# Performance work log

Measured on AMD Instinct MI355X. Metric: run time of the kernel, lower is better.

The kernel has to match this reference:

```python
import jax, jax.numpy as jnp
import numpy as np

H = 16      # num_heads
D = 64      # head_dim
BQ = 64     # block_size_q
BKV = 64    # block_size_kv


def setup_inputs() -> dict:
    key = jax.random.key(0)
    ks = jax.random.split(key, 5)
    B, S, dim = 2, 2048, 1024
    x = jax.random.normal(ks[0], (B, S, dim), dtype=jnp.float32)
    Wq = jax.random.normal(ks[1], (dim, H * D), dtype=jnp.float32) * 0.02
    Wk = jax.random.normal(ks[2], (dim, H * D), dtype=jnp.float32) * 0.02
    Wv = jax.random.normal(ks[3], (dim, H * D), dtype=jnp.float32) * 0.02
    Wo = jax.random.normal(ks[4], (H * D, dim), dtype=jnp.float32) * 0.02
    return {"x": x, "Wq": Wq, "Wk": Wk, "Wv": Wv, "Wo": Wo}


def _flash_tiled(q, k, v, scale):
    # q,k,v: (B, H, S, D). Non-causal tiled attention with online softmax,
    # faithfully replicating the source's per-iteration division by l_new.
    B, nh, S, d = q.shape
    nq, nkv = S // BQ, S // BKV
    qb = q.reshape(B, nh, nq, BQ, d)                       # all q blocks at once (outer loop vectorized)
    kb = k.reshape(B, nh, nkv, BKV, d).transpose(2, 0, 1, 3, 4)  # (nkv, B, H, BKV, D)
    vb = v.reshape(B, nh, nkv, BKV, d).transpose(2, 0, 1, 3, 4)

    o0 = jnp.zeros((B, nh, nq, BQ, d), q.dtype)
    m0 = jnp.full((B, nh, nq, BQ), -jnp.inf, q.dtype)
    l0 = jnp.zeros((B, nh, nq, BQ), q.dtype)

    def step(carry, kv):
        o, m, l = carry
        kj, vj = kv
        s = jnp.einsum('bhnqd,bhkd->bhnqk', qb, kj) * scale   # (B,H,nq,BQ,BKV)
        m_new = jnp.maximum(m, s.max(axis=-1))
        p = jnp.exp(s - m_new[..., None])
        alpha = jnp.exp(m - m_new)
        l_new = alpha * l + p.sum(axis=-1)
        # NOTE: division by l_new every iteration, as in the source module.
        o_new = (alpha[..., None] * o + jnp.einsum('bhnqk,bhkd->bhnqd', p, vj)) / l_new[..., None]
        return (o_new, m_new, l_new), None

    (o, _, _), _ = jax.lax.scan(step, (o0, m0, l0), (kb, vb))
    return o.reshape(B, nh, S, d)


def reference(x, Wq, Wk, Wv, Wo):
    B, S, dim = x.shape
    scale = D ** -0.5
    q = (x @ Wq).reshape(B, S, H, D).transpose(0, 2, 1, 3)
    k = (x @ Wk).reshape(B, S, H, D).transpose(0, 2, 1, 3)
    v = (x @ Wv).reshape(B, S, H, D).transpose(0, 2, 1, 3)
    o = _flash_tiled(q, k, v, scale)                       # (B,H,S,D)
    out = o.transpose(0, 2, 1, 3).reshape(B, S, H * D)
    return out @ Wo
```

## Files before the change

kernel.cpp:

```cpp
#include <hip/hip_runtime.h>
#include <hip/hip_bf16.h>
#include <math.h>

#define BB   2
#define SS   2048
#define DIM  1024
#define NH   16
#define HD   64
#define MTOT (BB * SS)

typedef unsigned short ushortT;
typedef __attribute__((ext_vector_type(8))) short short8v;
typedef __attribute__((ext_vector_type(4))) float float4v;

union FragU { short8v v; unsigned short us[8]; unsigned int u[4]; };

__device__ inline unsigned short f2bf(float x) {
    unsigned u = __builtin_bit_cast(unsigned, x);
    u += 0x7fffu + ((u >> 16) & 1u);
    return (unsigned short)(u >> 16);
}
__device__ inline float bf2f(unsigned short h) {
    unsigned u = ((unsigned)h) << 16;
    return __builtin_bit_cast(float, u);
}
__device__ inline void split_tr(float x, unsigned short& hi, unsigned short& lo) {
    unsigned u = __builtin_bit_cast(unsigned, x);
    hi = (unsigned short)(u >> 16);
    float hf = __builtin_bit_cast(float, u & 0xffff0000u);
    lo = (unsigned short)(__builtin_bit_cast(unsigned, x - hf) >> 16);
}
__device__ inline void split4(const float4& x, short4& hi, short4& lo) {
    unsigned short h0 = f2bf(x.x), h1 = f2bf(x.y), h2 = f2bf(x.z), h3 = f2bf(x.w);
    hi = make_short4((short)h0, (short)h1, (short)h2, (short)h3);
    lo = make_short4((short)f2bf(x.x - bf2f(h0)), (short)f2bf(x.y - bf2f(h1)),
                     (short)f2bf(x.z - bf2f(h2)), (short)f2bf(x.w - bf2f(h3)));
}
__device__ inline void gld_lds16(const void* g, void* l) {
    __builtin_amdgcn_global_load_lds(
        (const __attribute__((address_space(1))) void*)g,
        (__attribute__((address_space(3))) void*)l, 16, 0, 0);
}

__global__ __launch_bounds__(256) void convert_split_kernel(
    const float* __restrict__ in, ushortT* __restrict__ hi, ushortT* __restrict__ lo, int n4)
{
    int t = blockIdx.x * 256 + threadIdx.x;
    if (t < n4) {
        float4 x = ((const float4*)in)[t];
        short4 h, l; split4(x, h, l);
        ((short4*)hi)[t] = h;
        ((short4*)lo)[t] = l;
    }
}

__global__ __launch_bounds__(256) void transpose_split_kernel(
    const float* __restrict__ W0, const float* __restrict__ W1,
    const float* __restrict__ W2, const float* __restrict__ W3,
    ushortT* __restrict__ WtH, ushortT* __restrict__ WtL)
{
    const int z = blockIdx.z;
    const float* __restrict__ W = (z == 0) ? W0 : (z == 1) ? W1 : (z == 2) ? W2 : W3;
    ushortT* H = WtH + (size_t)z * 1024 * 1024;
    ushortT* L = WtL + (size_t)z * 1024 * 1024;

    __shared__ float T[64][65];
    const int k0 = blockIdx.y * 64, n0 = blockIdx.x * 64;
    const int tid = threadIdx.x;
    const int c4 = (tid & 15) * 4;

#pragma unroll
    for (int i = 0; i < 4; i++) {
        int r = (tid >> 4) + 16 * i;
        *(float4*)&T[r][c4] = *(const float4*)(W + (size_t)(k0 + r) * 1024 + n0 + c4);
    }
    __syncthreads();
#pragma unroll
    for (int i = 0; i < 4; i++) {
        int n = (tid >> 4) + 16 * i;
        float4 vv = make_float4(T[c4 + 0][n], T[c4 + 1][n], T[c4 + 2][n], T[c4 + 3][n]);
        short4 h, l; split4(vv, h, l);
        *(short4*)&H[(size_t)(n0 + n) * 1024 + k0 + c4] = h;
        *(short4*)&L[(size_t)(n0 + n) * 1024 + k0 + c4] = l;
    }
}

__global__ __launch_bounds__(256) void kv_convert_kernel(
    const float* __restrict__ kw,
    ushortT* __restrict__ KhG, ushortT* __restrict__ KlG)
{
    const int jb = blockIdx.x, bh = blockIdx.y;
    const int b = bh >> 4, h = bh & 15;

    __shared__ float T[64][68];
    const int tid = threadIdx.x;
    const size_t ibase = (size_t)b * SS * DIM + (size_t)h * HD + (size_t)(jb * 64) * DIM;
    const int c4 = (tid & 15) * 4;
#pragma unroll
    for (int i = 0; i < 4; i++) {
        int r = (tid >> 4) + 16 * i;
        *(float4*)&T[r][c4] = *(const float4*)(kw + ibase + (size_t)r * DIM + c4);
    }
    __syncthreads();

    ushortT* oh = KhG + (size_t)(bh * 32 + jb) * 4096;
    ushortT* ol = KlG + (size_t)(bh * 32 + jb) * 4096;

#pragma unroll
    for (int i = 0; i < 2; i++) {
        const int s = tid + i * 256;
        const int f = s >> 6;
        const int lane = s & 63;
        const int ks = f >> 2, c = f & 3;
        const int qd = lane >> 4, l15 = lane & 15;
        const int kv = c * 16 + l15;
        const int d0 = ks * 32 + qd * 8;
        ushortT hv[8], lv[8];
#pragma unroll
        for (int j = 0; j < 8; j++) split_tr(T[kv][d0 + j], hv[j], lv[j]);
        *(short4*)&oh[s * 8]     = *(short4*)&hv[0];
        *(short4*)&oh[s * 8 + 4] = *(short4*)&hv[4];
        *(short4*)&ol[s * 8]     = *(short4*)&lv[0];
        *(short4*)&ol[s * 8 + 4] = *(short4*)&lv[4];
    }
}

__global__ __launch_bounds__(256, 3) void gemm_bt_split_kernel(
    const ushortT* __restrict__ Ah, const ushortT* __restrict__ Al,
    const ushortT* __restrict__ BtH, const ushortT* __restrict__ BtL,
    float* __restrict__ Y0, float* __restrict__ Y1,
    ushortT* __restrict__ VhG, ushortT* __restrict__ VlG)
{
    const int z = blockIdx.z;
    const ushortT* __restrict__ Bh = BtH + (size_t)z * 1024 * 1024;
    const ushortT* __restrict__ Bl = BtL + (size_t)z * 1024 * 1024;

    const int K = 1024, N = 1024;
    const int m0 = blockIdx.y * 128;
    const int n0 = blockIdx.x * 128;

    __shared__ __align__(16) ushortT AhS[128 * 32];
    __shared__ __align__(16) ushortT AlS[128 * 32];
    __shared__ __align__(16) ushortT BhS[128 * 32];
    __shared__ __align__(16) ushortT BlS[128 * 32];

    const int tid  = threadIdx.x;
    const int wave = tid >> 6, lane = tid & 63;
    const int quad = lane >> 4, l15 = lane & 15;
    const int wm = wave >> 1, wn = wave & 1;

    const int s0 = tid, s1 = tid + 256;
    const int ar0 = s0 >> 2, ak0 = (s0 & 3) * 8;
    const int ar1 = s1 >> 2, ak1 = (s1 & 3) * 8;

    float4v acc[4][4];
#pragma unroll
    for (int i = 0; i < 4; i++)
#pragma unroll
        for (int j = 0; j < 4; j++) acc[i][j] = (float4v){0.f, 0.f, 0.f, 0.f};

    for (int k0 = 0; k0 < K; k0 += 32) {
        __syncthreads();
        gld_lds16(Ah + (size_t)(m0 + ar0) * K + k0 + ak0, &AhS[s0 * 8]);
        gld_lds16(Ah + (size_t)(m0 + ar1) * K + k0 + ak1, &AhS[s1 * 8]);
        gld_lds16(Al + (size_t)(m0 + ar0) * K + k0 + ak0, &AlS[s0 * 8]);
        gld_lds16(Al + (size_t)(m0 + ar1) * K + k0 + ak1, &AlS[s1 * 8]);
        gld_lds16(Bh + (size_t)(n0 + ar0) * K + k0 + ak0, &BhS[s0 * 8]);
        gld_lds16(Bh + (size_t)(n0 + ar1) * K + k0 + ak1, &BhS[s1 * 8]);
        gld_lds16(Bl + (size_t)(n0 + ar0) * K + k0 + ak0, &BlS[s0 * 8]);
        gld_lds16(Bl + (size_t)(n0 + ar1) * K + k0 + ak1, &BlS[s1 * 8]);
        __syncthreads();

        FragU ah[4], al[4], bh[4], bl[4];
#pragma unroll
        for (int t = 0; t < 4; t++) {
            ah[t].v = *(const short8v*)&AhS[(wm * 64 + t * 16 + l15) * 32 + quad * 8];
            al[t].v = *(const short8v*)&AlS[(wm * 64 + t * 16 + l15) * 32 + quad * 8];
            bh[t].v = *(const short8v*)&BhS[(wn * 64 + t * 16 + l15) * 32 + quad * 8];
            bl[t].v = *(const short8v*)&BlS[(wn * 64 + t * 16 + l15) * 32 + quad * 8];
        }
#pragma unroll
        for (int mt = 0; mt < 4; mt++)
#pragma unroll
            for (int nt = 0; nt < 4; nt++) {
                acc[mt][nt] = __builtin_amdgcn_mfma_f32_16x16x32_bf16(ah[mt].v, bh[nt].v, acc[mt][nt], 0, 0, 0);
                acc[mt][nt] = __builtin_amdgcn_mfma_f32_16x16x32_bf16(ah[mt].v, bl[nt].v, acc[mt][nt], 0, 0, 0);
                acc[mt][nt] = __builtin_amdgcn_mfma_f32_16x16x32_bf16(al[mt].v, bh[nt].v, acc[mt][nt], 0, 0, 0);
            }
    }

    if (z == 2) {
        const int b  = m0 >> 11;
        const int jb = ((m0 & 2047) >> 6) + wm;
        const int h  = (n0 >> 6) + wn;
        const size_t tb = (size_t)((b * 16 + h) * 32 + jb) * 4096;
        ushortT* vh = VhG + tb;
        ushortT* vl = VlG + tb;
#pragma unroll
        for (int mt = 0; mt < 4; mt++)
#pragma unroll
            for (int nt = 0; nt < 4; nt++) {
                const int off = ((((mt >> 1) * 4 + nt) * 64 +
                                  ((mt & 1) * 2 + (quad >> 1)) * 16 + l15) * 8) +
                                (quad & 1) * 4;
                short4 hi, lo;
                float4 vv = make_float4(acc[mt][nt][0], acc[mt][nt][1],
                                        acc[mt][nt][2], acc[mt][nt][3]);
                unsigned short h0, l0, h1, l1, h2, l2, h3, l3;
                split_tr(vv.x, h0, l0); split_tr(vv.y, h1, l1);
                split_tr(vv.z, h2, l2); split_tr(vv.w, h3, l3);
                hi = make_short4((short)h0, (short)h1, (short)h2, (short)h3);
                lo = make_short4((short)l0, (short)l1, (short)l2, (short)l3);
                *(short4*)&vh[off] = hi;
                *(short4*)&vl[off] = lo;
            }
    } else {
        float* __restrict__ Y = (z == 0) ? Y0 : Y1;
#pragma unroll
        for (int mt = 0; mt < 4; mt++)
#pragma unroll
            for (int r = 0; r < 4; r++) {
                const int row = m0 + wm * 64 + mt * 16 + quad * 4 + r;
                float* yp = Y + (size_t)row * N + n0 + wn * 64 + l15;
#pragma unroll
                for (int nt = 0; nt < 4; nt++)
                    yp[nt * 16] = acc[mt][nt][r];
            }
    }
}

__global__ __launch_bounds__(256, 2) void attn_mfma_kernel(
    const float* __restrict__ q,
    const ushortT* __restrict__ KhG, const ushortT* __restrict__ KlG,
    const ushortT* __restrict__ VhG, const ushortT* __restrict__ VlG,
    ushortT* __restrict__ Oh, ushortT* __restrict__ Ol)
{
    __shared__ __align__(16) ushortT KhS[4096];
    __shared__ __align__(16) ushortT KlS[4096];
    __shared__ __align__(16) ushortT VhS[4096];
    __shared__ __align__(16) ushortT VlS[4096];
    __shared__ __align__(16) ushortT PW[4][2][2048];

    const int tid  = threadIdx.x;
    const int wave = tid >> 6, lane = tid & 63;
    const int quad = lane >> 4, l15 = lane & 15;
    const int bh = blockIdx.y, b = bh >> 4, h = bh & 15;
    const size_t base = (size_t)b * SS * DIM + (size_t)h * HD;
    const int qs0 = blockIdx.x * 128 + wave * 32;

    const float qscale = 0.125f * 1.4426950408889634f;
    FragU Qh[2][2], Ql[2][2];
#pragma unroll
    for (int rt = 0; rt < 2; rt++) {
        const int qrow = qs0 + rt * 16 + l15;
#pragma unroll
        for (int ks = 0; ks < 2; ks++) {
            const float* p0 = q + base + (size_t)qrow * DIM + ks * 32 + quad * 8;
            float4 a = *(const float4*)(p0);
            float4 c = *(const float4*)(p0 + 4);
            float e[8] = {a.x, a.y, a.z, a.w, c.x, c.y, c.z, c.w};
#pragma unroll
            for (int j = 0; j < 8; j++) {
                float x = e[j] * qscale;
                unsigned short hs = f2bf(x);
                Qh[rt][ks].us[j] = hs;
                Ql[rt][ks].us[j] = f2bf(x - bf2f(hs));
            }
        }
    }

    float4v Oacc[4][2];
#pragma unroll
    for (int dt = 0; dt < 4; dt++)
#pragma unroll
        for (int rt = 0; rt < 2; rt++) Oacc[dt][rt] = (float4v){0.f, 0.f, 0.f, 0.f};

    float m_run[2] = {-INFINITY, -INFINITY};
    float l_run[2] = {0.f, 0.f};

    const int sl0 = wave * 128 + lane, sl1 = sl0 + 64;
    ushortT* ph = &PW[wave][0][0];
    ushortT* pl = &PW[wave][1][0];
    const int pwq = ((quad >> 1) * 16 + l15) * 8 + (quad & 1) * 4;
    const int lane8 = lane * 8;

    for (int jb = 0; jb < 32; jb++) {
        __syncthreads();
        {
            const size_t tb = (size_t)(bh * 32 + jb) * 4096;
            gld_lds16(KhG + tb + sl0 * 8, &KhS[sl0 * 8]);
            gld_lds16(KhG + tb + sl1 * 8, &KhS[sl1 * 8]);
            gld_lds16(KlG + tb + sl0 * 8, &KlS[sl0 * 8]);
            gld_lds16(KlG + tb + sl1 * 8, &KlS[sl1 * 8]);
            gld_lds16(VhG + tb + sl0 * 8, &VhS[sl0 * 8]);
            gld_lds16(VhG + tb + sl1 * 8, &VhS[sl1 * 8]);
            gld_lds16(VlG + tb + sl0 * 8, &VlS[sl0 * 8]);
            gld_lds16(VlG + tb + sl1 * 8, &VlS[sl1 * 8]);
        }
        __syncthreads();

        float4v st[4][2];
#pragma unroll
        for (int mt = 0; mt < 4; mt++)
#pragma unroll
            for (int rt = 0; rt < 2; rt++) st[mt][rt] = (float4v){0.f, 0.f, 0.f, 0.f};

#pragma unroll
        for (int ks = 0; ks < 2; ks++) {
            FragU kh[4], kl[4];
#pragma unroll
            for (int mt = 0; mt < 4; mt++) {
                kh[mt].v = *(const short8v*)&KhS[((ks * 4 + mt) * 64) * 8 + lane8];
                kl[mt].v = *(const short8v*)&KlS[((ks * 4 + mt) * 64) * 8 + lane8];
            }
#pragma unroll
            for (int mt = 0; mt < 4; mt++)
#pragma unroll
                for (int rt = 0; rt < 2; rt++) {
                    st[mt][rt] = __builtin_amdgcn_mfma_f32_16x16x32_bf16(kh[mt].v, Qh[rt][ks].v, st[mt][rt], 0, 0, 0);
                    st[mt][rt] = __builtin_amdgcn_mfma_f32_16x16x32_bf16(kh[mt].v, Ql[rt][ks].v, st[mt][rt], 0, 0, 0);
                    st[mt][rt] = __builtin_amdgcn_mfma_f32_16x16x32_bf16(kl[mt].v, Qh[rt][ks].v, st[mt][rt], 0, 0, 0);
                }
        }

        float oscale[2];
#pragma unroll
        for (int rt = 0; rt < 2; rt++) {
            float v0 = fmaxf(fmaxf(st[0][rt][0], st[0][rt][1]), fmaxf(st[0][rt][2], st[0][rt][3]));
#pragma unroll
            for (int mt = 1; mt < 4; mt++) {
                float v1 = fmaxf(fmaxf(st[mt][rt][0], st[mt][rt][1]), fmaxf(st[mt][rt][2], st[mt][rt][3]));
                v0 = fmaxf(v0, v1);
            }
            v0 = fmaxf(v0, __shfl_xor(v0, 16, 64));
            v0 = fmaxf(v0, __shfl_xor(v0, 32, 64));
            const float mn = fmaxf(m_run[rt], v0);
            const float al = __builtin_amdgcn_exp2f(m_run[rt] - mn);

            float ssum = 0.f;
#pragma unroll
            for (int mt = 0; mt < 4; mt++)
#pragma unroll
                for (int r = 0; r < 4; r++) {
                    const float p = __builtin_amdgcn_exp2f(st[mt][rt][r] - mn);
                    st[mt][rt][r] = p;
                    ssum += p;
                }
            ssum += __shfl_xor(ssum, 16, 64);
            ssum += __shfl_xor(ssum, 32, 64);
            const float ln = al * l_run[rt] + ssum;
            const float inv = __builtin_amdgcn_rcpf(ln);
            oscale[rt] = al * inv;
#pragma unroll
            for (int mt = 0; mt < 4; mt++)
#pragma unroll
                for (int r = 0; r < 4; r++)
                    st[mt][rt][r] *= inv;
            m_run[rt] = mn;
            l_run[rt] = ln;
        }

#pragma unroll
        for (int rt = 0; rt < 2; rt++)
#pragma unroll
            for (int mt = 0; mt < 4; mt++) {
                unsigned u0 = __builtin_bit_cast(unsigned, st[mt][rt][0]);
                unsigned u1 = __builtin_bit_cast(unsigned, st[mt][rt][1]);
                unsigned u2 = __builtin_bit_cast(unsigned, st[mt][rt][2]);
                unsigned u3 = __builtin_bit_cast(unsigned, st[mt][rt][3]);
                unsigned h01 = (u0 >> 16) | (u1 & 0xffff0000u);
                unsigned h23 = (u2 >> 16) | (u3 & 0xffff0000u);
                float d0 = st[mt][rt][0] - __builtin_bit_cast(float, u0 & 0xffff0000u);
                float d1 = st[mt][rt][1] - __builtin_bit_cast(float, u1 & 0xffff0000u);
                float d2 = st[mt][rt][2] - __builtin_bit_cast(float, u2 & 0xffff0000u);
                float d3 = st[mt][rt][3] - __builtin_bit_cast(float, u3 & 0xffff0000u);
                unsigned l01 = (__builtin_bit_cast(unsigned, d0) >> 16) |
                               (__builtin_bit_cast(unsigned, d1) & 0xffff0000u);
                unsigned l23 = (__builtin_bit_cast(unsigned, d2) >> 16) |
                               (__builtin_bit_cast(unsigned, d3) & 0xffff0000u);
                const int idx = ((rt * 2 + (mt >> 1)) * 512 + (mt & 1) * 256) + pwq;
                *(uint2*)&ph[idx] = make_uint2(h01, h23);
                *(uint2*)&pl[idx] = make_uint2(l01, l23);
            }

        FragU Ph[2][2], Pl[2][2];
#pragma unroll
        for (int rt = 0; rt < 2; rt++)
#pragma unroll
            for (int ks = 0; ks < 2; ks++) {
                Ph[rt][ks].v = *(const short8v*)&ph[((rt * 2 + ks) * 64) * 8 + lane8];
                Pl[rt][ks].v = *(const short8v*)&pl[((rt * 2 + ks) * 64) * 8 + lane8];
            }

#pragma unroll
        for (int dt = 0; dt < 4; dt++)
#pragma unroll
            for (int rt = 0; rt < 2; rt++)
#pragma unroll
                for (int r = 0; r < 4; r++)
                    Oacc[dt][rt][r] *= oscale[rt];

#pragma unroll
        for (int ks = 0; ks < 2; ks++)
#pragma unroll
            for (int dt = 0; dt < 4; dt++) {
                FragU vh, vl;
                vh.v = *(const short8v*)&VhS[((ks * 4 + dt) * 64) * 8 + lane8];
                vl.v = *(const short8v*)&VlS[((ks * 4 + dt) * 64) * 8 + lane8];
#pragma unroll
                for (int rt = 0; rt < 2; rt++) {
                    Oacc[dt][rt] = __builtin_amdgcn_mfma_f32_16x16x32_bf16(vh.v, Ph[rt][ks].v, Oacc[dt][rt], 0, 0, 0);
                    Oacc[dt][rt] = __builtin_amdgcn_mfma_f32_16x16x32_bf16(vl.v, Ph[rt][ks].v, Oacc[dt][rt], 0, 0, 0);
                    Oacc[dt][rt] = __builtin_amdgcn_mfma_f32_16x16x32_bf16(vh.v, Pl[rt][ks].v, Oacc[dt][rt], 0, 0, 0);
                }
            }
    }

    float* Pf = (float*)&PW[wave][0][0];
    const int q16 = lane >> 2, c = lane & 3;
#pragma unroll
    for (int rt = 0; rt < 2; rt++) {
#pragma unroll
        for (int dt = 0; dt < 4; dt++)
            *(float4v*)&Pf[l15 * 68 + dt * 16 + quad * 4] = Oacc[dt][rt];
        float vals[16];
#pragma unroll
        for (int kk = 0; kk < 4; kk++)
            *(float4v*)&vals[kk * 4] = *(const float4v*)&Pf[q16 * 68 + c * 16 + kk * 4];

        unsigned ho[8], lo8[8];
#pragma unroll
        for (int kk = 0; kk < 8; kk++) {
            unsigned short h0, l0, h1, l1;
            split_tr(vals[2 * kk], h0, l0);
            split_tr(vals[2 * kk + 1], h1, l1);
            ho[kk]  = (unsigned)h0 | ((unsigned)h1 << 16);
            lo8[kk] = (unsigned)l0 | ((unsigned)l1 << 16);
        }
        const int qrow = qs0 + rt * 16 + q16;
        const size_t off = (size_t)(b * SS + qrow) * DIM + h * HD + c * 16;
        *(uint4*)&Oh[off]     = make_uint4(ho[0], ho[1], ho[2], ho[3]);
        *(uint4*)&Oh[off + 8] = make_uint4(ho[4], ho[5], ho[6], ho[7]);
        *(uint4*)&Ol[off]     = make_uint4(lo8[0], lo8[1], lo8[2], lo8[3]);
        *(uint4*)&Ol[off + 8] = make_uint4(lo8[4], lo8[5], lo8[6], lo8[7]);
    }
}

extern "C" void kernel_launch(void* const* d_in, const int* in_sizes, int n_in,
                              void* d_out, int out_size, void* d_ws, size_t ws_size,
                              hipStream_t stream)
{
    const float* x  = (const float*)d_in[0];
    const float* Wq = (const float*)d_in[1];
    const float* Wk = (const float*)d_in[2];
    const float* Wv = (const float*)d_in[3];
    const float* Wo = (const float*)d_in[4];
    float* out = (float*)d_out;

    char* w = (char*)d_ws;
    float*   qw  = (float*)(w);
    float*   kw  = (float*)(w + ((size_t)16 << 20));
    ushortT* VhG = (ushortT*)(w + ((size_t)32 << 20));
    ushortT* VlG = (ushortT*)(w + ((size_t)40 << 20));
    ushortT* XhS = (ushortT*)(w + ((size_t)48 << 20));
    ushortT* XlS = (ushortT*)(w + ((size_t)56 << 20));
    ushortT* WtH = (ushortT*)(w + ((size_t)64 << 20));
    ushortT* WtL = (ushortT*)(w + ((size_t)72 << 20));
    ushortT* KhG = (ushortT*)(w + ((size_t)80 << 20));
    ushortT* KlG = (ushortT*)(w + ((size_t)88 << 20));
    ushortT* OhS = (ushortT*)kw;
    ushortT* OlS = (ushortT*)(w + ((size_t)24 << 20));

    dim3 blk(256);
    const int n4 = MTOT * DIM / 4;

    convert_split_kernel<<<dim3(n4 / 256), blk, 0, stream>>>(x, XhS, XlS, n4);
    transpose_split_kernel<<<dim3(16, 16, 4), blk, 0, stream>>>(Wq, Wk, Wv, Wo, WtH, WtL);

    gemm_bt_split_kernel<<<dim3(8, 32, 3), blk, 0, stream>>>(
        XhS, XlS, WtH, WtL, qw, kw, VhG, VlG);

    kv_convert_kernel<<<dim3(32, 32), blk, 0, stream>>>(kw, KhG, KlG);

    attn_mfma_kernel<<<dim3(16, 32), blk, 0, stream>>>(qw, KhG, KlG, VhG, VlG, OhS, OlS);

    gemm_bt_split_kernel<<<dim3(8, 32, 1), blk, 0, stream>>>(
        OhS, OlS, WtH + (size_t)3 * 1024 * 1024, WtL + (size_t)3 * 1024 * 1024,
        out, nullptr, nullptr, nullptr);
}
```

Baseline: 333.5 us.

## Fuse K split into projection GEMM, merge prep kernels, prefetch K/V tiles

Merges the x-convert and weight-transpose kernels into one launch. Moves the K hi/lo split and fragment relayout into the QKV GEMM epilogue, using swapped MFMA operands for z==1, so the separate kv_convert kernel and the fp32 K round trip through memory go away. In the attention loop, K and V fragments are loaded into registers before a barrier, and the next tile's global-to-LDS loads are issued so they overlap the current compute. This adds register pressure and extra barriers in exchange for fewer launches, less memory traffic and latency hiding.

Measured after the change: 780.7 us. 2.34x slower.

```diff
diff --git a/kernel.cpp b/kernel.cpp
--- a/kernel.cpp
+++ b/kernel.cpp
@@ -42,31 +42,29 @@
         (__attribute__((address_space(3))) void*)l, 16, 0, 0);
 }
 
-__global__ __launch_bounds__(256) void convert_split_kernel(
-    const float* __restrict__ in, ushortT* __restrict__ hi, ushortT* __restrict__ lo, int n4)
-{
-    int t = blockIdx.x * 256 + threadIdx.x;
-    if (t < n4) {
-        float4 x = ((const float4*)in)[t];
-        short4 h, l; split4(x, h, l);
-        ((short4*)hi)[t] = h;
-        ((short4*)lo)[t] = l;
-    }
-}
-
-__global__ __launch_bounds__(256) void transpose_split_kernel(
+__global__ __launch_bounds__(256) void prep_kernel(
+    const float* __restrict__ x,
     const float* __restrict__ W0, const float* __restrict__ W1,
     const float* __restrict__ W2, const float* __restrict__ W3,
+    ushortT* __restrict__ XhS, ushortT* __restrict__ XlS,
     ushortT* __restrict__ WtH, ushortT* __restrict__ WtL)
 {
     const int z = blockIdx.z;
+    const int tid = threadIdx.x;
+    if (z >= 4) {
+        int t = (((z - 4) * 256 + blockIdx.y * 16 + blockIdx.x)) * 256 + tid;
+        float4 xv = ((const float4*)x)[t];
+        short4 h, l; split4(xv, h, l);
+        ((short4*)XhS)[t] = h;
+        ((short4*)XlS)[t] = l;
+        return;
+    }
     const float* __restrict__ W = (z == 0) ? W0 : (z == 1) ? W1 : (z == 2) ? W2 : W3;
     ushortT* H = WtH + (size_t)z * 1024 * 1024;
     ushortT* L = WtL + (size_t)z * 1024 * 1024;
 
     __shared__ float T[64][65];
     const int k0 = blockIdx.y * 64, n0 = blockIdx.x * 64;
-    const int tid = threadIdx.x;
     const int c4 = (tid & 15) * 4;
 
 #pragma unroll
@@ -85,50 +83,11 @@
     }
 }
 
-__global__ __launch_bounds__(256) void kv_convert_kernel(
-    const float* __restrict__ kw,
-    ushortT* __restrict__ KhG, ushortT* __restrict__ KlG)
-{
-    const int jb = blockIdx.x, bh = blockIdx.y;
-    const int b = bh >> 4, h = bh & 15;
-
-    __shared__ float T[64][68];
-    const int tid = threadIdx.x;
-    const size_t ibase = (size_t)b * SS * DIM + (size_t)h * HD + (size_t)(jb * 64) * DIM;
-    const int c4 = (tid & 15) * 4;
-#pragma unroll
-    for (int i = 0; i < 4; i++) {
-        int r = (tid >> 4) + 16 * i;
-        *(float4*)&T[r][c4] = *(const float4*)(kw + ibase + (size_t)r * DIM + c4);
-    }
-    __syncthreads();
-
-    ushortT* oh = KhG + (size_t)(bh * 32 + jb) * 4096;
-    ushortT* ol = KlG + (size_t)(bh * 32 + jb) * 4096;
-
-#pragma unroll
-    for (int i = 0; i < 2; i++) {
-        const int s = tid + i * 256;
-        const int f = s >> 6;
-        const int lane = s & 63;
-        const int ks = f >> 2, c = f & 3;
-        const int qd = lane >> 4, l15 = lane & 15;
-        const int kv = c * 16 + l15;
-        const int d0 = ks * 32 + qd * 8;
-        ushortT hv[8], lv[8];
-#pragma unroll
-        for (int j = 0; j < 8; j++) split_tr(T[kv][d0 + j], hv[j], lv[j]);
-        *(short4*)&oh[s * 8]     = *(short4*)&hv[0];
-        *(short4*)&oh[s * 8 + 4] = *(short4*)&hv[4];
-        *(short4*)&ol[s * 8]     = *(short4*)&lv[0];
-        *(short4*)&ol[s * 8 + 4] = *(short4*)&lv[4];
-    }
-}
-
 __global__ __launch_bounds__(256, 3) void gemm_bt_split_kernel(
     const ushortT* __restrict__ Ah, const ushortT* __restrict__ Al,
     const ushortT* __restrict__ BtH, const ushortT* __restrict__ BtL,
-    float* __restrict__ Y0, float* __restrict__ Y1,
+    float* __restrict__ Y0,
+    ushortT* __restrict__ KhG, ushortT* __restrict__ KlG,
     ushortT* __restrict__ VhG, ushortT* __restrict__ VlG)
 {
     const int z = blockIdx.z;
@@ -179,17 +138,48 @@
             bh[t].v = *(const short8v*)&BhS[(wn * 64 + t * 16 + l15) * 32 + quad * 8];
             bl[t].v = *(const short8v*)&BlS[(wn * 64 + t * 16 + l15) * 32 + quad * 8];
         }
+        if (z == 1) {
+#pragma unroll
+            for (int mt = 0; mt < 4; mt++)
+#pragma unroll
+                for (int nt = 0; nt < 4; nt++) {
+                    acc[mt][nt] = __builtin_amdgcn_mfma_f32_16x16x32_bf16(bh[nt].v, ah[mt].v, acc[mt][nt], 0, 0, 0);
+                    acc[mt][nt] = __builtin_amdgcn_mfma_f32_16x16x32_bf16(bh[nt].v, al[mt].v, acc[mt][nt], 0, 0, 0);
+                    acc[mt][nt] = __builtin_amdgcn_mfma_f32_16x16x32_bf16(bl[nt].v, ah[mt].v, acc[mt][nt], 0, 0, 0);
+                }
+        } else {
+#pragma unroll
+            for (int mt = 0; mt < 4; mt++)
+#pragma unroll
+                for (int nt = 0; nt < 4; nt++) {
+                    acc[mt][nt] = __builtin_amdgcn_mfma_f32_16x16x32_bf16(ah[mt].v, bh[nt].v, acc[mt][nt], 0, 0, 0);
+                    acc[mt][nt] = __builtin_amdgcn_mfma_f32_16x16x32_bf16(ah[mt].v, bl[nt].v, acc[mt][nt], 0, 0, 0);
+                    acc[mt][nt] = __builtin_amdgcn_mfma_f32_16x16x32_bf16(al[mt].v, bh[nt].v, acc[mt][nt], 0, 0, 0);
+                }
+        }
+    }
+
+    if (z == 1) {
+        const int b  = m0 >> 11;
+        const int jb = ((m0 & 2047) >> 6) + wm;
+        const int h  = (n0 >> 6) + wn;
+        const size_t tb = (size_t)((b * 16 + h) * 32 + jb) * 4096;
+        ushortT* kh = KhG + tb;
+        ushortT* kl = KlG + tb;
 #pragma unroll
         for (int mt = 0; mt < 4; mt++)
 #pragma unroll
             for (int nt = 0; nt < 4; nt++) {
-                acc[mt][nt] = __builtin_amdgcn_mfma_f32_16x16x32_bf16(ah[mt].v, bh[nt].v, acc[mt][nt], 0, 0, 0);
-                acc[mt][nt] = __builtin_amdgcn_mfma_f32_16x16x32_bf16(ah[mt].v, bl[nt].v, acc[mt][nt], 0, 0, 0);
-                acc[mt][nt] = __builtin_amdgcn_mfma_f32_16x16x32_bf16(al[mt].v, bh[nt].v, acc[mt][nt], 0, 0, 0);
-            }
-    }
-
-    if (z == 2) {
+                const int off = (((nt >> 1) * 4 + mt) * 64 +
+                                 (((2 * nt + (quad >> 1)) & 3) * 16 + l15)) * 8 +
+                                (quad & 1) * 4;
+                unsigned short h0, l0, h1, l1, h2, l2, h3, l3;
+                split_tr(acc[mt][nt][0], h0, l0); split_tr(acc[mt][nt][1], h1, l1);
+                split_tr(acc[mt][nt][2], h2, l2); split_tr(acc[mt][nt][3], h3, l3);
+                *(short4*)&kh[off] = make_short4((short)h0, (short)h1, (short)h2, (short)h3);
+                *(short4*)&kl[off] = make_short4((short)l0, (short)l1, (short)l2, (short)l3);
+            }
+    } else if (z == 2) {
         const int b  = m0 >> 11;
         const int jb = ((m0 & 2047) >> 6) + wm;
         const int h  = (n0 >> 6) + wn;
@@ -203,25 +193,19 @@
                 const int off = ((((mt >> 1) * 4 + nt) * 64 +
                                   ((mt & 1) * 2 + (quad >> 1)) * 16 + l15) * 8) +
                                 (quad & 1) * 4;
-                short4 hi, lo;
-                float4 vv = make_float4(acc[mt][nt][0], acc[mt][nt][1],
-                                        acc[mt][nt][2], acc[mt][nt][3]);
                 unsigned short h0, l0, h1, l1, h2, l2, h3, l3;
-                split_tr(vv.x, h0, l0); split_tr(vv.y, h1, l1);
-                split_tr(vv.z, h2, l2); split_tr(vv.w, h3, l3);
-                hi = make_short4((short)h0, (short)h1, (short)h2, (short)h3);
-                lo = make_short4((short)l0, (short)l1, (short)l2, (short)l3);
-                *(short4*)&vh[off] = hi;
-                *(short4*)&vl[off] = lo;
+                split_tr(acc[mt][nt][0], h0, l0); split_tr(acc[mt][nt][1], h1, l1);
+                split_tr(acc[mt][nt][2], h2, l2); split_tr(acc[mt][nt][3], h3, l3);
+                *(short4*)&vh[off] = make_short4((short)h0, (short)h1, (short)h2, (short)h3);
+                *(short4*)&vl[off] = make_short4((short)l0, (short)l1, (short)l2, (short)l3);
             }
     } else {
-        float* __restrict__ Y = (z == 0) ? Y0 : Y1;
 #pragma unroll
         for (int mt = 0; mt < 4; mt++)
 #pragma unroll
             for (int r = 0; r < 4; r++) {
                 const int row = m0 + wm * 64 + mt * 16 + quad * 4 + r;
-                float* yp = Y + (size_t)row * N + n0 + wn * 64 + l15;
+                float* yp = Y0 + (size_t)row * N + n0 + wn * 64 + l15;
 #pragma unroll
                 for (int nt = 0; nt < 4; nt++)
                     yp[nt * 16] = acc[mt][nt][r];
@@ -261,10 +245,10 @@
             float e[8] = {a.x, a.y, a.z, a.w, c.x, c.y, c.z, c.w};
 #pragma unroll
             for (int j = 0; j < 8; j++) {
-                float x = e[j] * qscale;
-                unsigned short hs = f2bf(x);
+                float xj = e[j] * qscale;
+                unsigned short hs = f2bf(xj);
                 Qh[rt][ks].us[j] = hs;
-                Ql[rt][ks].us[j] = f2bf(x - bf2f(hs));
+                Ql[rt][ks].us[j] = f2bf(xj - bf2f(hs));
             }
         }
     }
@@ -284,20 +268,37 @@
     const int pwq = ((quad >> 1) * 16 + l15) * 8 + (quad & 1) * 4;
     const int lane8 = lane * 8;
 
+    {
+        const size_t tb = (size_t)(bh * 32) * 4096;
+        gld_lds16(KhG + tb + sl0 * 8, &KhS[sl0 * 8]);
+        gld_lds16(KhG + tb + sl1 * 8, &KhS[sl1 * 8]);
+        gld_lds16(KlG + tb + sl0 * 8, &KlS[sl0 * 8]);
+        gld_lds16(KlG + tb + sl1 * 8, &KlS[sl1 * 8]);
+        gld_lds16(VhG + tb + sl0 * 8, &VhS[sl0 * 8]);
+        gld_lds16(VhG + tb + sl1 * 8, &VhS[sl1 * 8]);
+        gld_lds16(VlG + tb + sl0 * 8, &VlS[sl0 * 8]);
+        gld_lds16(VlG + tb + sl1 * 8, &VlS[sl1 * 8]);
+    }
+
     for (int jb = 0; jb < 32; jb++) {
+        const size_t tbn = (size_t)(bh * 32 + jb + 1) * 4096;
         __syncthreads();
-        {
-            const size_t tb = (size_t)(bh * 32 + jb) * 4096;
-            gld_lds16(KhG + tb + sl0 * 8, &KhS[sl0 * 8]);
-            gld_lds16(KhG + tb + sl1 * 8, &KhS[sl1 * 8]);
-            gld_lds16(KlG + tb + sl0 * 8, &KlS[sl0 * 8]);
-            gld_lds16(KlG + tb + sl1 * 8, &KlS[sl1 * 8]);
-            gld_lds16(VhG + tb + sl0 * 8, &VhS[sl0 * 8]);
-            gld_lds16(VhG + tb + sl1 * 8, &VhS[sl1 * 8]);
-            gld_lds16(VlG + tb + sl0 * 8, &VlS[sl0 * 8]);
-            gld_lds16(VlG + tb + sl1 * 8, &VlS[sl1 * 8]);
-        }
+
+        FragU kh[2][4], kl[2][4];
+#pragma unroll
+        for (int ks = 0; ks < 2; ks++)
+#pragma unroll
+            for (int mt = 0; mt < 4; mt++) {
+                kh[ks][mt].v = *(const short8v*)&KhS[((ks * 4 + mt) * 64) * 8 + lane8];
+                kl[ks][mt].v = *(const short8v*)&KlS[((ks * 4 + mt) * 64) * 8 + lane8];
+            }
         __syncthreads();
+        if (jb < 31) {
+            gld_lds16(KhG + tbn + sl0 * 8, &KhS[sl0 * 8]);
+            gld_lds16(KhG + tbn + sl1 * 8, &KhS[sl1 * 8]);
+            gld_lds16(KlG + tbn + sl0 * 8, &KlS[sl0 * 8]);
+            gld_lds16(KlG + tbn + sl1 * 8, &KlS[sl1 * 8]);
+        }
 
         float4v st[4][2];
 #pragma unroll
@@ -306,22 +307,15 @@
             for (int rt = 0; rt < 2; rt++) st[mt][rt] = (float4v){0.f, 0.f, 0.f, 0.f};
 
 #pragma unroll
-        for (int ks = 0; ks < 2; ks++) {
-            FragU kh[4], kl[4];
-#pragma unroll
-            for (int mt = 0; mt < 4; mt++) {
-                kh[mt].v = *(const short8v*)&KhS[((ks * 4 + mt) * 64) * 8 + lane8];
-                kl[mt].v = *(const short8v*)&KlS[((ks * 4 + mt) * 64) * 8 + lane8];
-            }
+        for (int ks = 0; ks < 2; ks++)
 #pragma unroll
             for (int mt = 0; mt < 4; mt++)
 #pragma unroll
                 for (int rt = 0; rt < 2; rt++) {
-                    st[mt][rt] = __builtin_amdgcn_mfma_f32_16x16x32_bf16(kh[mt].v, Qh[rt][ks].v, st[mt][rt], 0, 0, 0);
-                    st[mt][rt] = __builtin_amdgcn_mfma_f32_16x16x32_bf16(kh[mt].v, Ql[rt][ks].v, st[mt][rt], 0, 0, 0);
-                    st[mt][rt] = __builtin_amdgcn_mfma_f32_16x16x32_bf16(kl[mt].v, Qh[rt][ks].v, st[mt][rt], 0, 0, 0);
+                    st[mt][rt] = __builtin_amdgcn_mfma_f32_16x16x32_bf16(kh[ks][mt].v, Qh[rt][ks].v, st[mt][rt], 0, 0, 0);
+                    st[mt][rt] = __builtin_amdgcn_mfma_f32_16x16x32_bf16(kh[ks][mt].v, Ql[rt][ks].v, st[mt][rt], 0, 0, 0);
+                    st[mt][rt] = __builtin_amdgcn_mfma_f32_16x16x32_bf16(kl[ks][mt].v, Qh[rt][ks].v, st[mt][rt], 0, 0, 0);
                 }
-        }
 
         float oscale[2];
 #pragma unroll
@@ -392,6 +386,22 @@
                 Pl[rt][ks].v = *(const short8v*)&pl[((rt * 2 + ks) * 64) * 8 + lane8];
             }
 
+        FragU vh[2][4], vl[2][4];
+#pragma unroll
+        for (int ks = 0; ks < 2; ks++)
+#pragma unroll
+            for (int dt = 0; dt < 4; dt++) {
+                vh[ks][dt].v = *(const short8v*)&VhS[((ks * 4 + dt) * 64) * 8 + lane8];
+                vl[ks][dt].v = *(const short8v*)&VlS[((ks * 4 + dt) * 64) * 8 + lane8];
+            }
+        __syncthreads();
+        if (jb < 31) {
+            gld_lds16(VhG + tbn + sl0 * 8, &VhS[sl0 * 8]);
+            gld_lds16(VhG + tbn + sl1 * 8, &VhS[sl1 * 8]);
+            gld_lds16(VlG + tbn + sl0 * 8, &VlS[sl0 * 8]);
+            gld_lds16(VlG + tbn + sl1 * 8, &VlS[sl1 * 8]);
+        }
+
 #pragma unroll
         for (int dt = 0; dt < 4; dt++)
 #pragma unroll
@@ -403,17 +413,13 @@
 #pragma unroll
         for (int ks = 0; ks < 2; ks++)
 #pragma unroll
-            for (int dt = 0; dt < 4; dt++) {
-                FragU vh, vl;
-                vh.v = *(const short8v*)&VhS[((ks * 4 + dt) * 64) * 8 + lane8];
-                vl.v = *(const short8v*)&VlS[((ks * 4 + dt) * 64) * 8 + lane8];
+            for (int dt = 0; dt < 4; dt++)
 #pragma unroll
                 for (int rt = 0; rt < 2; rt++) {
-                    Oacc[dt][rt] = __builtin_amdgcn_mfma_f32_16x16x32_bf16(vh.v, Ph[rt][ks].v, Oacc[dt][rt], 0, 0, 0);
-                    Oacc[dt][rt] = __builtin_amdgcn_mfma_f32_16x16x32_bf16(vl.v, Ph[rt][ks].v, Oacc[dt][rt], 0, 0, 0);
-                    Oacc[dt][rt] = __builtin_amdgcn_mfma_f32_16x16x32_bf16(vh.v, Pl[rt][ks].v, Oacc[dt][rt], 0, 0, 0);
+                    Oacc[dt][rt] = __builtin_amdgcn_mfma_f32_16x16x32_bf16(vh[ks][dt].v, Ph[rt][ks].v, Oacc[dt][rt], 0, 0, 0);
+                    Oacc[dt][rt] = __builtin_amdgcn_mfma_f32_16x16x32_bf16(vl[ks][dt].v, Ph[rt][ks].v, Oacc[dt][rt], 0, 0, 0);
+                    Oacc[dt][rt] = __builtin_amdgcn_mfma_f32_16x16x32_bf16(vh[ks][dt].v, Pl[rt][ks].v, Oacc[dt][rt], 0, 0, 0);
                 }
-            }
     }
 
     float* Pf = (float*)&PW[wave][0][0];
@@ -459,7 +465,8 @@
 
     char* w = (char*)d_ws;
     float*   qw  = (float*)(w);
-    float*   kw  = (float*)(w + ((size_t)16 << 20));
+    ushortT* OhS = (ushortT*)(w + ((size_t)16 << 20));
+    ushortT* OlS = (ushortT*)(w + ((size_t)24 << 20));
     ushortT* VhG = (ushortT*)(w + ((size_t)32 << 20));
     ushortT* VlG = (ushortT*)(w + ((size_t)40 << 20));
     ushortT* XhS = (ushortT*)(w + ((size_t)48 << 20));
@@ -468,23 +475,18 @@
     ushortT* WtL = (ushortT*)(w + ((size_t)72 << 20));
     ushortT* KhG = (ushortT*)(w + ((size_t)80 << 20));
     ushortT* KlG = (ushortT*)(w + ((size_t)88 << 20));
-    ushortT* OhS = (ushortT*)kw;
-    ushortT* OlS = (ushortT*)(w + ((size_t)24 << 20));
 
     dim3 blk(256);
-    const int n4 = MTOT * DIM / 4;
-
-    convert_split_kernel<<<dim3(n4 / 256), blk, 0, stream>>>(x, XhS, XlS, n4);
-    transpose_split_kernel<<<dim3(16, 16, 4), blk, 0, stream>>>(Wq, Wk, Wv, Wo, WtH, WtL);
+
+    prep_kernel<<<dim3(16, 16, 20), blk, 0, stream>>>(
+        x, Wq, Wk, Wv, Wo, XhS, XlS, WtH, WtL);
 
     gemm_bt_split_kernel<<<dim3(8, 32, 3), blk, 0, stream>>>(
-        XhS, XlS, WtH, WtL, qw, kw, VhG, VlG);
-
-    kv_convert_kernel<<<dim3(32, 32), blk, 0, stream>>>(kw, KhG, KlG);
+        XhS, XlS, WtH, WtL, qw, KhG, KlG, VhG, VlG);
 
     attn_mfma_kernel<<<dim3(16, 32), blk, 0, stream>>>(qw, KhG, KlG, VhG, VlG, OhS, OlS);
 
     gemm_bt_split_kernel<<<dim3(8, 32, 1), blk, 0, stream>>>(
         OhS, OlS, WtH + (size_t)3 * 1024 * 1024, WtL + (size_t)3 * 1024 * 1024,
-        out, nullptr, nullptr, nullptr);
-}
+        out, nullptr, nullptr, nullptr, nullptr);
+}
```
